# Performance work log

Measured on AMD Instinct MI355X. Metric: run time of the kernel, lower is better.

The kernel has to match this reference:

```python
import jax, jax.numpy as jnp
import numpy as np

D_MODEL = 1024
NUM_HEADS = 16
DEPTH = D_MODEL // NUM_HEADS


def setup_inputs() -> dict:
    key = jax.random.key(0)
    ks = jax.random.split(key, 12)
    B, S = 2, 2048
    s = 0.02
    return {
        "q": jax.random.normal(ks[0], (B, S, D_MODEL), dtype=jnp.float32),
        "k": jax.random.normal(ks[1], (B, S, D_MODEL), dtype=jnp.float32),
        "v": jax.random.normal(ks[2], (B, S, D_MODEL), dtype=jnp.float32),
        "mask": jnp.ones((B, 1, 1, S), dtype=bool),  # accepted but unused, as in source
        "wq": jax.random.normal(ks[3], (D_MODEL, D_MODEL), dtype=jnp.float32) * s,
        "bq": jnp.zeros((D_MODEL,), dtype=jnp.float32),
        "wk": jax.random.normal(ks[4], (D_MODEL, D_MODEL), dtype=jnp.float32) * s,
        "bk": jnp.zeros((D_MODEL,), dtype=jnp.float32),
        "wv": jax.random.normal(ks[5], (D_MODEL, D_MODEL), dtype=jnp.float32) * s,
        "bv": jnp.zeros((D_MODEL,), dtype=jnp.float32),
        "wo": jax.random.normal(ks[6], (D_MODEL, D_MODEL), dtype=jnp.float32) * s,
        "bo": jnp.zeros((D_MODEL,), dtype=jnp.float32),
    }


def _split_heads(x, B):
    # [B, S, d_model] -> [B, H, S, depth]
    return x.reshape(B, -1, NUM_HEADS, DEPTH).transpose(0, 2, 1, 3)


def reference(q, k, v, mask, wq, bq, wk, bk, wv, bv, wo, bo):
    B = q.shape[0]
    qh = _split_heads(q @ wq + bq, B)  # [B,H,Sq,depth]
    kh = _split_heads(k @ wk + bk, B)  # [B,H,Sk,depth]
    vh = _split_heads(v @ wv + bv, B)  # [B,H,Sk,depth]
    scale = 1.0 / jnp.sqrt(jnp.asarray(DEPTH, dtype=qh.dtype))
    scores = jnp.einsum("bhqd,bhkd->bhqk", qh, kh) * scale  # [B,H,Sq,Sk]
    attn = jax.nn.softmax(scores, axis=-1)
    ctx = jnp.einsum("bhqk,bhkd->bhqd", attn, vh)  # [B,H,Sq,depth]
    concat = ctx.transpose(0, 2, 1, 3).reshape(B, -1, D_MODEL)  # [B,Sq,d_model]
    out = concat @ wo + bo
    return (out, attn)
```

## Files before the change

kernel.cpp:

```cpp
#include <hip/hip_runtime.h>
#include <hip/hip_bf16.h>
#include <cstdint>
#include <cstddef>

#define BATCH 2
#define SEQ 2048
#define NH 16
#define DH 64
#define DM 1024
#define MTOT 4096

typedef __attribute__((ext_vector_type(8))) short short8;
typedef __attribute__((ext_vector_type(4))) float f32x4;

#define MFMA16(a, b, c) __builtin_amdgcn_mfma_f32_16x16x32_bf16((a), (b), (c), 0, 0, 0)

__device__ __forceinline__ unsigned short f2bf(float f) {
  unsigned int u = __builtin_bit_cast(unsigned int, f);
  u += 0x7fffu + ((u >> 16) & 1u);
  return (unsigned short)(u >> 16);
}

__global__ __launch_bounds__(256) void cvt_x(const float* __restrict__ q,
                                             const float* __restrict__ k,
                                             const float* __restrict__ v,
                                             unsigned short* __restrict__ dst) {
  const float* srcs[3] = {q, k, v};
  const float* s = srcs[blockIdx.y];
  unsigned short* d = dst + (size_t)blockIdx.y * (MTOT * DM);
  int i = blockIdx.x * 256 + threadIdx.x;
  if (i < (MTOT * DM / 4)) {
    float4 f = ((const float4*)s)[i];
    ushort4 o;
    o.x = f2bf(f.x); o.y = f2bf(f.y); o.z = f2bf(f.z); o.w = f2bf(f.w);
    ((ushort4*)d)[i] = o;
  }
}

__global__ __launch_bounds__(256) void cvt_w(const float* __restrict__ w0,
                                             const float* __restrict__ w1,
                                             const float* __restrict__ w2,
                                             const float* __restrict__ w3,
                                             unsigned short* __restrict__ dst) {
  const float* srcs[4] = {w0, w1, w2, w3};
  const float* src = srcs[blockIdx.z];
  unsigned short* d = dst + (size_t)blockIdx.z * (DM * DM);
  __shared__ float t[32][33];
  int tx = threadIdx.x & 31, ty = threadIdx.x >> 5;
  int k0 = blockIdx.y * 32, n0 = blockIdx.x * 32;
#pragma unroll
  for (int r = 0; r < 32; r += 8) t[ty + r][tx] = src[(k0 + ty + r) * DM + n0 + tx];
  __syncthreads();
#pragma unroll
  for (int r = 0; r < 32; r += 8) d[(n0 + ty + r) * DM + k0 + tx] = f2bf(t[tx][ty + r]);
}

template <int MODE>
__global__ __launch_bounds__(256) void gemm128(const unsigned short* __restrict__ A,
                                               const unsigned short* __restrict__ Bt,
                                               const float* __restrict__ bias,
                                               void* __restrict__ out) {
  __shared__ unsigned short As[128 * 32];
  __shared__ unsigned short Bs[128 * 32];
  int tid = threadIdx.x, lane = tid & 63;
  int w = tid >> 6, wm = (w >> 1) * 64, wn = (w & 1) * 64;
  int quad = lane >> 4, l15 = lane & 15;
  int m0 = blockIdx.x * 128, n0 = blockIdx.y * 128;
  f32x4 acc[4][4] = {};

  int r0 = tid >> 2;
  int c0 = (tid & 3) * 8;
  const uint4* ga0 = (const uint4*)(A + (size_t)(m0 + r0) * DM + c0);
  const uint4* ga1 = (const uint4*)(A + (size_t)(m0 + 64 + r0) * DM + c0);
  const uint4* gb0 = (const uint4*)(Bt + (size_t)(n0 + r0) * DM + c0);
  const uint4* gb1 = (const uint4*)(Bt + (size_t)(n0 + 64 + r0) * DM + c0);

  for (int k0 = 0; k0 < DM; k0 += 32) {
    uint4 va0 = ga0[k0 >> 3];
    uint4 va1 = ga1[k0 >> 3];
    uint4 vb0 = gb0[k0 >> 3];
    uint4 vb1 = gb1[k0 >> 3];
    __syncthreads();
    *(uint4*)(As + tid * 8) = va0;
    *(uint4*)(As + 2048 + tid * 8) = va1;
    *(uint4*)(Bs + tid * 8) = vb0;
    *(uint4*)(Bs + 2048 + tid * 8) = vb1;
    __syncthreads();
    short8 af[4], bfr[4];
#pragma unroll
    for (int t = 0; t < 4; t++) {
      af[t] = *(const short8*)(As + (wm + t * 16 + l15) * 32 + quad * 8);
      bfr[t] = *(const short8*)(Bs + (wn + t * 16 + l15) * 32 + quad * 8);
    }
#pragma unroll
    for (int i = 0; i < 4; i++)
#pragma unroll
      for (int j = 0; j < 4; j++) acc[i][j] = MFMA16(af[i], bfr[j], acc[i][j]);
  }

  float bvals[4];
#pragma unroll
  for (int j = 0; j < 4; j++) bvals[j] = bias[n0 + wn + j * 16 + l15];
#pragma unroll
  for (int i = 0; i < 4; i++) {
#pragma unroll
    for (int j = 0; j < 4; j++) {
#pragma unroll
      for (int r = 0; r < 4; r++) {
        int m = m0 + wm + i * 16 + quad * 4 + r;
        int n = n0 + wn + j * 16 + l15;
        float v = acc[i][j][r] + bvals[j];
        if (MODE == 0) {
          unsigned short* dq = (unsigned short*)out;
          dq[(((size_t)((m >> 11) * 16 + (n >> 6)) * SEQ + (m & 2047)) * DH) + (n & 63)] = f2bf(v);
        } else if (MODE == 1) {
          unsigned short* dq = (unsigned short*)out;
          dq[(((size_t)((m >> 11) * 16 + (n >> 6)) * DH + (n & 63)) * SEQ) + (m & 2047)] = f2bf(v);
        } else {
          ((float*)out)[(size_t)m * DM + n] = v;
        }
      }
    }
  }
}

__global__ __launch_bounds__(256) void attn_fused(const unsigned short* __restrict__ Qh,
                                                  const unsigned short* __restrict__ Kh,
                                                  const unsigned short* __restrict__ VhT,
                                                  float* __restrict__ attn_out,
                                                  unsigned short* __restrict__ ctx) {
  int bh = blockIdx.x;
  int q0 = blockIdx.y * 64;
  int tid = threadIdx.x, w = tid >> 6, lane = tid & 63;
  int quad = lane >> 4, l15 = lane & 15;
  int qrow = q0 + w * 16;
  const unsigned short* Qb = Qh + ((size_t)bh * SEQ + qrow) * DH;
  const unsigned short* Kb = Kh + (size_t)bh * SEQ * DH;
  const unsigned short* Vb = VhT + (size_t)bh * DH * SEQ;

  short8 aq0 = *(const short8*)(Qb + l15 * DH + quad * 8);
  short8 aq1 = *(const short8*)(Qb + l15 * DH + 32 + quad * 8);

  float part[4] = {0.f, 0.f, 0.f, 0.f};
  for (int kt = 0; kt < SEQ; kt += 16) {
    const unsigned short* kp = Kb + (size_t)(kt + l15) * DH + quad * 8;
    short8 bk0 = *(const short8*)(kp);
    short8 bk1 = *(const short8*)(kp + 32);
    f32x4 s = {0.f, 0.f, 0.f, 0.f};
    s = MFMA16(aq0, bk0, s);
    s = MFMA16(aq1, bk1, s);
#pragma unroll
    for (int r = 0; r < 4; r++) part[r] += __expf(s[r] * 0.125f);
  }
#pragma unroll
  for (int off = 1; off < 16; off <<= 1) {
#pragma unroll
    for (int r = 0; r < 4; r++) part[r] += __shfl_xor(part[r], off, 64);
  }
  float inv[4];
#pragma unroll
  for (int r = 0; r < 4; r++) inv[r] = 1.0f / part[r];

  __shared__ unsigned short plds[4][16 * 40];
  unsigned short* pl = &plds[w][0];
  f32x4 cacc[4] = {};
  float* arow = attn_out + ((size_t)bh * SEQ + qrow) * SEQ;

  for (int kt = 0; kt < SEQ; kt += 32) {
#pragma unroll
    for (int t = 0; t < 2; t++) {
      int kc = kt + t * 16;
      const unsigned short* kp = Kb + (size_t)(kc + l15) * DH + quad * 8;
      short8 bk0 = *(const short8*)(kp);
      short8 bk1 = *(const short8*)(kp + 32);
      f32x4 s = {0.f, 0.f, 0.f, 0.f};
      s = MFMA16(aq0, bk0, s);
      s = MFMA16(aq1, bk1, s);
#pragma unroll
      for (int r = 0; r < 4; r++) {
        float p = __expf(s[r] * 0.125f) * inv[r];
        arow[(size_t)(quad * 4 + r) * SEQ + kc + l15] = p;
        pl[(quad * 4 + r) * 40 + t * 16 + l15] = f2bf(p);
      }
    }
    short8 pa = *(const short8*)(pl + l15 * 40 + quad * 8);
#pragma unroll
    for (int dt = 0; dt < 4; dt++) {
      short8 bv = *(const short8*)(Vb + (size_t)(dt * 16 + l15) * SEQ + kt + quad * 8);
      cacc[dt] = MFMA16(pa, bv, cacc[dt]);
    }
  }

  int b = bh >> 4, h = bh & 15;
#pragma unroll
  for (int dt = 0; dt < 4; dt++) {
#pragma unroll
    for (int r = 0; r < 4; r++) {
      int m = b * SEQ + qrow + quad * 4 + r;
      int c = h * DH + dt * 16 + l15;
      ctx[(size_t)m * DM + c] = f2bf(cacc[dt][r]);
    }
  }
}

extern "C" void kernel_launch(void* const* d_in, const int* in_sizes, int n_in,
                              void* d_out, int out_size, void* d_ws, size_t ws_size,
                              hipStream_t stream) {
  const float* q  = (const float*)d_in[0];
  const float* k  = (const float*)d_in[1];
  const float* v  = (const float*)d_in[2];
  const float* wq = (const float*)d_in[4];
  const float* bq = (const float*)d_in[5];
  const float* wk = (const float*)d_in[6];
  const float* bk = (const float*)d_in[7];
  const float* wv = (const float*)d_in[8];
  const float* bv = (const float*)d_in[9];
  const float* wo = (const float*)d_in[10];
  const float* bo = (const float*)d_in[11];

  char* ws = (char*)d_ws;
  unsigned short* xb  = (unsigned short*)(ws);
  unsigned short* wT  = (unsigned short*)(ws + (size_t)24 * 1024 * 1024);
  unsigned short* QH  = (unsigned short*)(ws + (size_t)32 * 1024 * 1024);
  unsigned short* KH  = (unsigned short*)(ws + (size_t)40 * 1024 * 1024);
  unsigned short* VT  = (unsigned short*)(ws + (size_t)48 * 1024 * 1024);
  unsigned short* CTX = (unsigned short*)(ws + (size_t)56 * 1024 * 1024);

  float* out_proj = (float*)d_out;
  float* attn_out = (float*)d_out + (size_t)MTOT * DM;

  cvt_x<<<dim3(MTOT * DM / 4 / 256, 3), 256, 0, stream>>>(q, k, v, xb);
  cvt_w<<<dim3(32, 32, 4), 256, 0, stream>>>(wq, wk, wv, wo, wT);

  gemm128<0><<<dim3(32, 8), 256, 0, stream>>>(xb, wT, bq, QH);
  gemm128<0><<<dim3(32, 8), 256, 0, stream>>>(xb + (size_t)MTOT * DM, wT + (size_t)DM * DM, bk, KH);
  gemm128<1><<<dim3(32, 8), 256, 0, stream>>>(xb + (size_t)2 * MTOT * DM, wT + (size_t)2 * DM * DM, bv, VT);

  attn_fused<<<dim3(BATCH * NH, SEQ / 64), 256, 0, stream>>>(QH, KH, VT, attn_out, CTX);

  gemm128<2><<<dim3(32, 8), 256, 0, stream>>>(CTX, wT + (size_t)3 * DM * DM, bo, out_proj);
}
```

Baseline: 995.4 us.

## Batch QKV GEMMs, shrink tiles, and coalesce attention-probability stores via LDS

Merges the three Q/K/V projection GEMMs into one launch over a z-dimension and shrinks the GEMM tile to 128x64 to get more blocks. The attention kernel drops to 2 waves per block (32 query rows), processes 32 keys per iteration, and prefetches V fragments early. Probabilities are staged in fp32 LDS and written to the large attn output as coalesced 16-byte nontemporal stores rather than scattered scalar stores. The trade-off is more LDS traffic and lower per-block reuse in the GEMMs.

```diff
diff --git a/kernel.cpp b/kernel.cpp
--- a/kernel.cpp
+++ b/kernel.cpp
@@ -55,82 +55,88 @@
   for (int r = 0; r < 32; r += 8) d[(n0 + ty + r) * DM + k0 + tx] = f2bf(t[tx][ty + r]);
 }
 
-template <int MODE>
-__global__ __launch_bounds__(256) void gemm128(const unsigned short* __restrict__ A,
-                                               const unsigned short* __restrict__ Bt,
-                                               const float* __restrict__ bias,
-                                               void* __restrict__ out) {
+template <int KIND>
+__global__ __launch_bounds__(256) void gemm_t64(const unsigned short* __restrict__ Abase,
+                                                const unsigned short* __restrict__ Wbase,
+                                                const float* __restrict__ b0,
+                                                const float* __restrict__ b1,
+                                                const float* __restrict__ b2,
+                                                void* __restrict__ outbase) {
+  const int z = (KIND == 0) ? blockIdx.z : 0;
+  const unsigned short* A = Abase + (size_t)z * MTOT * DM;
+  const unsigned short* Bt = Wbase + (size_t)z * DM * DM;
+  const float* bias = (KIND == 1) ? b0 : (z == 0 ? b0 : (z == 1 ? b1 : b2));
+
   __shared__ unsigned short As[128 * 32];
-  __shared__ unsigned short Bs[128 * 32];
+  __shared__ unsigned short Bs[64 * 32];
   int tid = threadIdx.x, lane = tid & 63;
-  int w = tid >> 6, wm = (w >> 1) * 64, wn = (w & 1) * 64;
+  int w = tid >> 6;
   int quad = lane >> 4, l15 = lane & 15;
-  int m0 = blockIdx.x * 128, n0 = blockIdx.y * 128;
-  f32x4 acc[4][4] = {};
+  int m0 = blockIdx.x * 128, n0 = blockIdx.y * 64;
+  f32x4 acc[2][4] = {};
 
   int r0 = tid >> 2;
   int c0 = (tid & 3) * 8;
   const uint4* ga0 = (const uint4*)(A + (size_t)(m0 + r0) * DM + c0);
   const uint4* ga1 = (const uint4*)(A + (size_t)(m0 + 64 + r0) * DM + c0);
-  const uint4* gb0 = (const uint4*)(Bt + (size_t)(n0 + r0) * DM + c0);
-  const uint4* gb1 = (const uint4*)(Bt + (size_t)(n0 + 64 + r0) * DM + c0);
+  const uint4* gb  = (const uint4*)(Bt + (size_t)(n0 + r0) * DM + c0);
 
   for (int k0 = 0; k0 < DM; k0 += 32) {
     uint4 va0 = ga0[k0 >> 3];
     uint4 va1 = ga1[k0 >> 3];
-    uint4 vb0 = gb0[k0 >> 3];
-    uint4 vb1 = gb1[k0 >> 3];
+    uint4 vb  = gb[k0 >> 3];
     __syncthreads();
     *(uint4*)(As + tid * 8) = va0;
     *(uint4*)(As + 2048 + tid * 8) = va1;
-    *(uint4*)(Bs + tid * 8) = vb0;
-    *(uint4*)(Bs + 2048 + tid * 8) = vb1;
+    *(uint4*)(Bs + tid * 8) = vb;
     __syncthreads();
-    short8 af[4], bfr[4];
-#pragma unroll
-    for (int t = 0; t < 4; t++) {
-      af[t] = *(const short8*)(As + (wm + t * 16 + l15) * 32 + quad * 8);
-      bfr[t] = *(const short8*)(Bs + (wn + t * 16 + l15) * 32 + quad * 8);
-    }
-#pragma unroll
-    for (int i = 0; i < 4; i++)
+    short8 af[2], bfr[4];
+#pragma unroll
+    for (int i = 0; i < 2; i++)
+      af[i] = *(const short8*)(As + (w * 32 + i * 16 + l15) * 32 + quad * 8);
+#pragma unroll
+    for (int j = 0; j < 4; j++)
+      bfr[j] = *(const short8*)(Bs + (j * 16 + l15) * 32 + quad * 8);
+#pragma unroll
+    for (int i = 0; i < 2; i++)
 #pragma unroll
       for (int j = 0; j < 4; j++) acc[i][j] = MFMA16(af[i], bfr[j], acc[i][j]);
   }
 
   float bvals[4];
 #pragma unroll
-  for (int j = 0; j < 4; j++) bvals[j] = bias[n0 + wn + j * 16 + l15];
-#pragma unroll
-  for (int i = 0; i < 4; i++) {
+  for (int j = 0; j < 4; j++) bvals[j] = bias[n0 + j * 16 + l15];
+#pragma unroll
+  for (int i = 0; i < 2; i++) {
 #pragma unroll
     for (int j = 0; j < 4; j++) {
 #pragma unroll
       for (int r = 0; r < 4; r++) {
-        int m = m0 + wm + i * 16 + quad * 4 + r;
-        int n = n0 + wn + j * 16 + l15;
+        int m = m0 + w * 32 + i * 16 + quad * 4 + r;
+        int n = n0 + j * 16 + l15;
         float v = acc[i][j][r] + bvals[j];
-        if (MODE == 0) {
-          unsigned short* dq = (unsigned short*)out;
-          dq[(((size_t)((m >> 11) * 16 + (n >> 6)) * SEQ + (m & 2047)) * DH) + (n & 63)] = f2bf(v);
-        } else if (MODE == 1) {
-          unsigned short* dq = (unsigned short*)out;
-          dq[(((size_t)((m >> 11) * 16 + (n >> 6)) * DH + (n & 63)) * SEQ) + (m & 2047)] = f2bf(v);
+        if (KIND == 1) {
+          ((float*)outbase)[(size_t)m * DM + n] = v;
         } else {
-          ((float*)out)[(size_t)m * DM + n] = v;
+          unsigned short* dq = (unsigned short*)outbase + (size_t)z * MTOT * DM;
+          if (z < 2) {
+            dq[(((size_t)((m >> 11) * 16 + (n >> 6)) * SEQ + (m & 2047)) * DH) + (n & 63)] = f2bf(v);
+          } else {
+            dq[(((size_t)((m >> 11) * 16 + (n >> 6)) * DH + (n & 63)) * SEQ) + (m & 2047)] = f2bf(v);
+          }
         }
       }
     }
   }
 }
 
-__global__ __launch_bounds__(256) void attn_fused(const unsigned short* __restrict__ Qh,
+__global__ __launch_bounds__(128) void attn_fused(const unsigned short* __restrict__ Qh,
                                                   const unsigned short* __restrict__ Kh,
                                                   const unsigned short* __restrict__ VhT,
                                                   float* __restrict__ attn_out,
                                                   unsigned short* __restrict__ ctx) {
   int bh = blockIdx.x;
-  int q0 = blockIdx.y * 64;
+  int q0 = blockIdx.y * 32;
   int tid = threadIdx.x, w = tid >> 6, lane = tid & 63;
   int quad = lane >> 4, l15 = lane & 15;
   int qrow = q0 + w * 16;
@@ -142,15 +148,20 @@
   short8 aq1 = *(const short8*)(Qb + l15 * DH + 32 + quad * 8);
 
   float part[4] = {0.f, 0.f, 0.f, 0.f};
-  for (int kt = 0; kt < SEQ; kt += 16) {
+  for (int kt = 0; kt < SEQ; kt += 32) {
     const unsigned short* kp = Kb + (size_t)(kt + l15) * DH + quad * 8;
-    short8 bk0 = *(const short8*)(kp);
-    short8 bk1 = *(const short8*)(kp + 32);
-    f32x4 s = {0.f, 0.f, 0.f, 0.f};
-    s = MFMA16(aq0, bk0, s);
-    s = MFMA16(aq1, bk1, s);
-#pragma unroll
-    for (int r = 0; r < 4; r++) part[r] += __expf(s[r] * 0.125f);
+    short8 k00 = *(const short8*)(kp);
+    short8 k01 = *(const short8*)(kp + 32);
+    short8 k10 = *(const short8*)(kp + 16 * DH);
+    short8 k11 = *(const short8*)(kp + 16 * DH + 32);
+    f32x4 s0 = {0.f, 0.f, 0.f, 0.f}, s1 = {0.f, 0.f, 0.f, 0.f};
+    s0 = MFMA16(aq0, k00, s0);
+    s0 = MFMA16(aq1, k01, s0);
+    s1 = MFMA16(aq0, k10, s1);
+    s1 = MFMA16(aq1, k11, s1);
+#pragma unroll
+    for (int r = 0; r < 4; r++)
+      part[r] += __expf(s0[r] * 0.125f) + __expf(s1[r] * 0.125f);
   }
 #pragma unroll
   for (int off = 1; off < 16; off <<= 1) {
@@ -161,44 +172,64 @@
 #pragma unroll
   for (int r = 0; r < 4; r++) inv[r] = 1.0f / part[r];
 
-  __shared__ unsigned short plds[4][16 * 40];
-  unsigned short* pl = &plds[w][0];
-  f32x4 cacc[4] = {};
+  __shared__ float plds[2][16 * 36];
+  float* pl = &plds[w][0];
+  f32x4 cacc0 = {}, cacc1 = {}, cacc2 = {}, cacc3 = {};
   float* arow = attn_out + ((size_t)bh * SEQ + qrow) * SEQ;
 
   for (int kt = 0; kt < SEQ; kt += 32) {
-#pragma unroll
-    for (int t = 0; t < 2; t++) {
-      int kc = kt + t * 16;
-      const unsigned short* kp = Kb + (size_t)(kc + l15) * DH + quad * 8;
-      short8 bk0 = *(const short8*)(kp);
-      short8 bk1 = *(const short8*)(kp + 32);
-      f32x4 s = {0.f, 0.f, 0.f, 0.f};
-      s = MFMA16(aq0, bk0, s);
-      s = MFMA16(aq1, bk1, s);
-#pragma unroll
-      for (int r = 0; r < 4; r++) {
-        float p = __expf(s[r] * 0.125f) * inv[r];
-        arow[(size_t)(quad * 4 + r) * SEQ + kc + l15] = p;
-        pl[(quad * 4 + r) * 40 + t * 16 + l15] = f2bf(p);
-      }
-    }
-    short8 pa = *(const short8*)(pl + l15 * 40 + quad * 8);
-#pragma unroll
-    for (int dt = 0; dt < 4; dt++) {
-      short8 bv = *(const short8*)(Vb + (size_t)(dt * 16 + l15) * SEQ + kt + quad * 8);
-      cacc[dt] = MFMA16(pa, bv, cacc[dt]);
-    }
+    const unsigned short* vp = Vb + (size_t)l15 * SEQ + kt + quad * 8;
+    short8 bv0 = *(const short8*)(vp);
+    short8 bv1 = *(const short8*)(vp + 16 * SEQ);
+    short8 bv2 = *(const short8*)(vp + 32 * SEQ);
+    short8 bv3 = *(const short8*)(vp + 48 * SEQ);
+
+    const unsigned short* kp = Kb + (size_t)(kt + l15) * DH + quad * 8;
+    short8 k00 = *(const short8*)(kp);
+    short8 k01 = *(const short8*)(kp + 32);
+    short8 k10 = *(const short8*)(kp + 16 * DH);
+    short8 k11 = *(const short8*)(kp + 16 * DH + 32);
+    f32x4 s0 = {0.f, 0.f, 0.f, 0.f}, s1 = {0.f, 0.f, 0.f, 0.f};
+    s0 = MFMA16(aq0, k00, s0);
+    s0 = MFMA16(aq1, k01, s0);
+    s1 = MFMA16(aq0, k10, s1);
+    s1 = MFMA16(aq1, k11, s1);
+#pragma unroll
+    for (int r = 0; r < 4; r++) {
+      float p0 = __expf(s0[r] * 0.125f) * inv[r];
+      float p1 = __expf(s1[r] * 0.125f) * inv[r];
+      pl[(quad * 4 + r) * 36 + l15] = p0;
+      pl[(quad * 4 + r) * 36 + 16 + l15] = p1;
+    }
+    {
+      int rr = lane >> 3, cc = (lane & 7) * 4;
+      f32x4 row0 = *(const f32x4*)(pl + rr * 36 + cc);
+      f32x4 row1 = *(const f32x4*)(pl + (rr + 8) * 36 + cc);
+      __builtin_nontemporal_store(row0, (f32x4*)(arow + (size_t)rr * SEQ + kt + cc));
+      __builtin_nontemporal_store(row1, (f32x4*)(arow + (size_t)(rr + 8) * SEQ + kt + cc));
+    }
+    f32x4 pf0 = *(const f32x4*)(pl + l15 * 36 + quad * 8);
+    f32x4 pf1 = *(const f32x4*)(pl + l15 * 36 + quad * 8 + 4);
+    short8 pa;
+    pa[0] = (short)f2bf(pf0[0]); pa[1] = (short)f2bf(pf0[1]);
+    pa[2] = (short)f2bf(pf0[2]); pa[3] = (short)f2bf(pf0[3]);
+    pa[4] = (short)f2bf(pf1[0]); pa[5] = (short)f2bf(pf1[1]);
+    pa[6] = (short)f2bf(pf1[2]); pa[7] = (short)f2bf(pf1[3]);
+    cacc0 = MFMA16(pa, bv0, cacc0);
+    cacc1 = MFMA16(pa, bv1, cacc1);
+    cacc2 = MFMA16(pa, bv2, cacc2);
+    cacc3 = MFMA16(pa, bv3, cacc3);
   }
 
   int b = bh >> 4, h = bh & 15;
+  f32x4 cc[4] = {cacc0, cacc1, cacc2, cacc3};
 #pragma unroll
   for (int dt = 0; dt < 4; dt++) {
 #pragma unroll
     for (int r = 0; r < 4; r++) {
       int m = b * SEQ + qrow + quad * 4 + r;
       int c = h * DH + dt * 16 + l15;
-      ctx[(size_t)m * DM + c] = f2bf(cacc[dt][r]);
+      ctx[(size_t)m * DM + c] = f2bf(cc[dt][r]);
     }
   }
 }
@@ -232,11 +263,9 @@
   cvt_x<<<dim3(MTOT * DM / 4 / 256, 3), 256, 0, stream>>>(q, k, v, xb);
   cvt_w<<<dim3(32, 32, 4), 256, 0, stream>>>(wq, wk, wv, wo, wT);
 
-  gemm128<0><<<dim3(32, 8), 256, 0, stream>>>(xb, wT, bq, QH);
-  gemm128<0><<<dim3(32, 8), 256, 0, stream>>>(xb + (size_t)MTOT * DM, wT + (size_t)DM * DM, bk, KH);
-  gemm128<1><<<dim3(32, 8), 256, 0, stream>>>(xb + (size_t)2 * MTOT * DM, wT + (size_t)2 * DM * DM, bv, VT);
-
-  attn_fused<<<dim3(BATCH * NH, SEQ / 64), 256, 0, stream>>>(QH, KH, VT, attn_out, CTX);
-
-  gemm128<2><<<dim3(32, 8), 256, 0, stream>>>(CTX, wT + (size_t)3 * DM * DM, bo, out_proj);
-}
+  gemm_t64<0><<<dim3(32, 16, 3), 256, 0, stream>>>(xb, wT, bq, bk, bv, QH);
+
+  attn_fused<<<dim3(BATCH * NH, SEQ / 32), 128, 0, stream>>>(QH, KH, VT, attn_out, CTX);
+
+  gemm_t64<1><<<dim3(32, 16), 256, 0, stream>>>(CTX, wT + (size_t)3 * DM * DM, bo, bo, bo, out_proj);
+}
```

Result: faster. 938.4 us (-5.7%).
